# Kernel optimization log

Measured on AMD Instinct MI355X. Metric: run time of the kernel, lower is better.

## Reference

```python
import jax, jax.numpy as jnp
import numpy as np

NUM_USERS = 80000
NUM_ITEMS = 40000
NUM_NODES = NUM_USERS + NUM_ITEMS
LATENT_DIM = 64
N_LAYERS = 3
ALPHA = 0.8
E_POS = 3_000_000
E_NEG = 1_500_000
E_PATH = 2_000_000
N_PATHS = 6


def _make_edges(rng, n_edges, n_nodes):
    # sample keys, dedupe so COO is coalesced (distinct (row,col) pairs)
    keys = rng.integers(0, n_nodes * n_nodes, size=int(n_edges * 1.05), dtype=np.int64)
    keys = np.unique(keys)[:n_edges]
    assert keys.shape[0] == n_edges
    row = (keys // n_nodes).astype(np.int32)
    col = (keys % n_nodes).astype(np.int32)
    return row, col


def setup_inputs() -> dict:
    key = jax.random.key(0)
    k1, k2, k3, k4, k5 = jax.random.split(key, 5)
    rng = np.random.default_rng(0)

    pos_row, pos_col = _make_edges(rng, E_POS, NUM_NODES)
    neg_row, neg_col = _make_edges(rng, E_NEG, NUM_NODES)
    p_row, p_col = _make_edges(rng, E_PATH, NUM_NODES)

    # path membership counts: for each coalesced edge, how many times each of the
    # 6 path matrices contains it (0/1 here); at least one path per edge
    counts = (rng.random((E_PATH, N_PATHS)) < 0.5).astype(np.float32)
    empty = counts.sum(axis=1) == 0
    counts[empty, 0] = 1.0

    return {
        "user_emb": 0.1 * jax.random.normal(k1, (NUM_USERS, LATENT_DIM), jnp.float32),
        "item_emb": 0.1 * jax.random.normal(k2, (NUM_ITEMS, LATENT_DIM), jnp.float32),
        "theta": jnp.ones((N_PATHS,), jnp.float32) / N_PATHS,
        "pos_row": jnp.asarray(pos_row),
        "pos_col": jnp.asarray(pos_col),
        "pos_val": jax.random.uniform(k3, (E_POS,), jnp.float32, 0.01, 1.0),
        "neg_row": jnp.asarray(neg_row),
        "neg_col": jnp.asarray(neg_col),
        "neg_val": jax.random.uniform(k4, (E_NEG,), jnp.float32, 0.01, 1.0),
        "p_row": jnp.asarray(p_row),
        "p_col": jnp.asarray(p_col),
        "p_counts": jnp.asarray(counts),
    }


def _spmm(row, col, val, x, n_nodes):
    # y = A @ x with A given as COO edge list: gather + segment scatter-add
    return jax.ops.segment_sum(val[:, None] * x[col], row, num_segments=n_nodes)


def reference(user_emb, item_emb, theta, pos_row, pos_col, pos_val,
              neg_row, neg_col, neg_val, p_row, p_col, p_counts):
    n = NUM_NODES

    # ---- build path-weighted matrix (coalesce + sparse row softmax, eq.(2)) ----
    theta_w = jax.nn.softmax(theta)                 # [6]
    vals = p_counts @ theta_w                       # coalesced values per edge [E_path]
    exp_v = jnp.exp(vals)
    row_sums = jax.ops.segment_sum(exp_v, p_row, num_segments=n)
    soft_v = exp_v / (row_sums[p_row] + 1e-12)      # row-level sparse softmax

    # ---- PEE: E_0 = P @ all_emb ----
    all_emb = jnp.concatenate([user_emb, item_emb], axis=0)  # [N, D]
    e = _spmm(p_row, p_col, soft_v, all_emb, n)
    embs = [e]

    # ---- signed propagation ----
    for _ in range(N_LAYERS):
        e_pos = _spmm(pos_row, pos_col, pos_val, e, n)
        e_neg_a = _spmm(neg_row, neg_col, neg_val, e, n)
        e = e_pos + ALPHA * (e - e_neg_a)
        embs.append(e)

    light_out = jnp.mean(jnp.stack(embs, axis=1), axis=1)   # [N, D]
    users = light_out[:NUM_USERS]
    items = light_out[NUM_USERS:]
    return users, items
```

## Files before the change

### kernel.cpp

```cpp
#include <hip/hip_runtime.h>

#define NUM_USERS 80000
#define NUM_ITEMS 40000
#define NUM_NODES 120000
#define DIM 64
#define ALPHA_C 0.8f

typedef unsigned short u16;
typedef unsigned int u32;
typedef int   i2v __attribute__((ext_vector_type(2)));
typedef u32   u4v __attribute__((ext_vector_type(4)));
typedef float f4v __attribute__((ext_vector_type(4)));

__device__ __forceinline__ u16 f2bf(float f) {
    union { float f; u32 i; } v;
    v.f = f;
    u32 i = v.i;
    u32 r = (i + 0x7FFFu + ((i >> 16) & 1u)) >> 16;
    return (u16)r;
}
__device__ __forceinline__ float lo_bf(u32 u) { return __uint_as_float(u << 16); }
__device__ __forceinline__ float hi_bf(u32 u) { return __uint_as_float(u & 0xffff0000u); }

__device__ __forceinline__ void acc8(float* __restrict__ acc, float v, uint4 q) {
    const u32* p = (const u32*)&q;
#pragma unroll
    for (int k = 0; k < 4; ++k) {
        u32 u = p[k];
        acc[2 * k]     = fmaf(v, lo_bf(u), acc[2 * k]);
        acc[2 * k + 1] = fmaf(v, hi_bf(u), acc[2 * k + 1]);
    }
}

__device__ __forceinline__ uint4 ldrow(const u16* __restrict__ x, int c, int li) {
    return *((const uint4*)(x + (size_t)c * DIM) + li);
}

template <bool SUMV>
__device__ __forceinline__ void seg_pipe(const i2v* __restrict__ ep0,
                                         int start, int end,
                                         const u16* __restrict__ x,
                                         int li,
                                         float* __restrict__ acc,
                                         float* __restrict__ vsum) {
    const int n = end - start;
    const i2v* ep = ep0 + start;
    float s = 0.f;
    const int np = n >> 1;
    if (np >= 4) {
        i2v ea0 = ep[0], ea1 = ep[1];
        i2v eb0 = ep[2], eb1 = ep[3];
        i2v ec0 = ep[4], ec1 = ep[5];
        i2v ed0 = ep[6], ed1 = ep[7];
        uint4 xa0 = ldrow(x, ea0.x, li), xa1 = ldrow(x, ea1.x, li);
        uint4 xb0 = ldrow(x, eb0.x, li), xb1 = ldrow(x, eb1.x, li);
        for (int p = 4; p < np; ++p) {
            i2v ee0 = ep[2 * p];
            i2v ee1 = ep[2 * p + 1];
            uint4 xc0 = ldrow(x, ec0.x, li);
            uint4 xc1 = ldrow(x, ec1.x, li);
            float va0 = __int_as_float(ea0.y), va1 = __int_as_float(ea1.y);
            acc8(acc, va0, xa0);
            acc8(acc, va1, xa1);
            if (SUMV) s += va0 + va1;
            ea0 = eb0; ea1 = eb1; eb0 = ec0; eb1 = ec1;
            ec0 = ed0; ec1 = ed1; ed0 = ee0; ed1 = ee1;
            xa0 = xb0; xa1 = xb1; xb0 = xc0; xb1 = xc1;
        }
        uint4 xc0 = ldrow(x, ec0.x, li), xc1 = ldrow(x, ec1.x, li);
        uint4 xd0 = ldrow(x, ed0.x, li), xd1 = ldrow(x, ed1.x, li);
        {
            float va0 = __int_as_float(ea0.y), va1 = __int_as_float(ea1.y);
            acc8(acc, va0, xa0); acc8(acc, va1, xa1);
            if (SUMV) s += va0 + va1;
        }
        {
            float vb0 = __int_as_float(eb0.y), vb1 = __int_as_float(eb1.y);
            acc8(acc, vb0, xb0); acc8(acc, vb1, xb1);
            if (SUMV) s += vb0 + vb1;
        }
        {
            float vc0 = __int_as_float(ec0.y), vc1 = __int_as_float(ec1.y);
            acc8(acc, vc0, xc0); acc8(acc, vc1, xc1);
            if (SUMV) s += vc0 + vc1;
        }
        {
            float vd0 = __int_as_float(ed0.y), vd1 = __int_as_float(ed1.y);
            acc8(acc, vd0, xd0); acc8(acc, vd1, xd1);
            if (SUMV) s += vd0 + vd1;
        }
        if (n & 1) {
            i2v eq = ep[n - 1];
            float v = __int_as_float(eq.y);
            uint4 xq = ldrow(x, eq.x, li);
            acc8(acc, v, xq);
            if (SUMV) s += v;
        }
    } else {
        for (int e = 0; e < n; ++e) {
            i2v eq = ep[e];
            float v = __int_as_float(eq.y);
            uint4 xq = ldrow(x, eq.x, li);
            acc8(acc, v, xq);
            if (SUMV) s += v;
        }
    }
    if (SUMV) *vsum = s;
}

__global__ void k_expv_pack(const float* __restrict__ p_counts,
                            const float* __restrict__ theta,
                            const int* __restrict__ p_col,
                            i2v* __restrict__ pev, int E) {
    int i = blockIdx.x * blockDim.x + threadIdx.x;
    if (i >= E) return;
    float m = -1e30f;
    for (int k = 0; k < 6; ++k) m = fmaxf(m, theta[k]);
    float e[6];
    float s = 0.f;
    for (int k = 0; k < 6; ++k) { e[k] = expf(theta[k] - m); s += e[k]; }
    float w0 = e[0] / s, w1 = e[1] / s, w2 = e[2] / s,
          w3 = e[3] / s, w4 = e[4] / s, w5 = e[5] / s;
    const float* c = p_counts + (size_t)i * 6;
    float v = c[0] * w0 + c[1] * w1 + c[2] * w2 +
              c[3] * w3 + c[4] * w4 + c[5] * w5;
    i2v o;
    o.x = __builtin_nontemporal_load(p_col + i);
    o.y = __float_as_int(expf(v));
    __builtin_nontemporal_store(o, pev + i);
}

__device__ __forceinline__ int lower_bound_v(const int* __restrict__ rows,
                                             int nnz, int r) {
    int lo = 0, hi = nnz;
    while (lo < hi) {
        int mid = (lo + hi) >> 1;
        if (rows[mid] < r) lo = mid + 1; else hi = mid;
    }
    return lo;
}

__global__ void k_row_ptr4(const int* __restrict__ rows_a, int nnz_a, int* __restrict__ pa,
                           const int* __restrict__ rows_b, int nnz_b, int* __restrict__ pb,
                           const int* __restrict__ rows_c, int nnz_c, int* __restrict__ pc,
                           int* __restrict__ pm) {
    int t = blockIdx.x * blockDim.x + threadIdx.x;
    int which = t / (NUM_NODES + 1);
    int r = t - which * (NUM_NODES + 1);
    if (which == 0) pa[r] = lower_bound_v(rows_a, nnz_a, r);
    else if (which == 1) pb[r] = lower_bound_v(rows_b, nnz_b, r);
    else if (which == 2) pc[r] = lower_bound_v(rows_c, nnz_c, r);
    else if (which == 3) pm[r] = lower_bound_v(rows_a, nnz_a, r) +
                                 lower_bound_v(rows_b, nnz_b, r);
}

__global__ void k_cvt(const float* __restrict__ user_emb,
                      const float* __restrict__ item_emb,
                      u16* __restrict__ emb16) {
    int i = blockIdx.x * blockDim.x + threadIdx.x;
    size_t f = (size_t)i * 4;
    const size_t UTOT = (size_t)NUM_USERS * DIM;
    const size_t TOT = (size_t)NUM_NODES * DIM;
    if (f >= TOT) return;
    f4v v = (f < UTOT) ? __builtin_nontemporal_load((const f4v*)(user_emb + f))
                       : __builtin_nontemporal_load((const f4v*)(item_emb + (f - UTOT)));
    ushort4 o;
    o.x = f2bf(v.x); o.y = f2bf(v.y); o.z = f2bf(v.z); o.w = f2bf(v.w);
    *(ushort4*)(emb16 + f) = o;
}

__global__ void k_merge_e(const int* __restrict__ row_p, const int* __restrict__ col_p,
                          const float* __restrict__ val_p,
                          const int* __restrict__ row_n, const int* __restrict__ col_n,
                          const float* __restrict__ val_n,
                          const int* __restrict__ rp_p, const int* __restrict__ rp_n,
                          i2v* __restrict__ mev, int E_pos, int E_tot) {
    int g = blockIdx.x * blockDim.x + threadIdx.x;
    if (g >= E_tot) return;
    if (g < E_pos) {
        int r = __builtin_nontemporal_load(row_p + g);
        i2v e;
        e.x = __builtin_nontemporal_load(col_p + g);
        e.y = __float_as_int(__builtin_nontemporal_load(val_p + g));
        __builtin_nontemporal_store(e, mev + (size_t)g + rp_n[r]);
    } else {
        int i = g - E_pos;
        int r = __builtin_nontemporal_load(row_n + i);
        i2v e;
        e.x = __builtin_nontemporal_load(col_n + i);
        e.y = __float_as_int(-ALPHA_C * __builtin_nontemporal_load(val_n + i));
        __builtin_nontemporal_store(e, mev + (size_t)i + rp_p[r + 1]);
    }
}

__global__ void k_path(const u16* __restrict__ emb16,
                       const i2v* __restrict__ pev,
                       const int* __restrict__ rp,
                       u16* __restrict__ e0) {
    int t = blockIdx.x * blockDim.x + threadIdx.x;
    int row = t >> 3;
    if (row >= NUM_NODES) return;
    int li = threadIdx.x & 7;
    int start = rp[row], end = rp[row + 1];

    float acc[8];
#pragma unroll
    for (int k = 0; k < 8; ++k) acc[k] = 0.f;
    float s = 0.f;

    seg_pipe<true>(pev, start, end, emb16, li, acc, &s);

    float inv = 1.0f / (s + 1e-12f);
    u32 o[4];
#pragma unroll
    for (int k = 0; k < 4; ++k)
        o[k] = (u32)f2bf(acc[2 * k] * inv) | ((u32)f2bf(acc[2 * k + 1] * inv) << 16);
    *((uint4*)(e0 + (size_t)row * DIM) + li) = *(uint4*)o;
}

template <int FINAL>
__global__ void k_layer_t(const u16* __restrict__ e_in,
                          u16* __restrict__ e_out,
                          const u16* __restrict__ e0,
                          const u16* __restrict__ e1,
                          float* __restrict__ out,
                          const int* __restrict__ rp_m,
                          const i2v* __restrict__ mev) {
    int t = blockIdx.x * blockDim.x + threadIdx.x;
    int row = t >> 3;
    if (row >= NUM_NODES) return;
    int li = threadIdx.x & 7;

    uint4 eq = *((const uint4*)(e_in + (size_t)row * DIM) + li);

    float acc[8];
#pragma unroll
    for (int k = 0; k < 8; ++k) acc[k] = 0.f;

    seg_pipe<false>(mev, rp_m[row], rp_m[row + 1], e_in, li, acc, nullptr);

    const u32* ep_ = (const u32*)&eq;
    float res[8];
#pragma unroll
    for (int k = 0; k < 4; ++k) {
        res[2 * k]     = acc[2 * k]     + ALPHA_C * lo_bf(ep_[k]);
        res[2 * k + 1] = acc[2 * k + 1] + ALPHA_C * hi_bf(ep_[k]);
    }

    if (FINAL) {
        u4v q0 = __builtin_nontemporal_load((const u4v*)(e0 + (size_t)row * DIM) + li);
        u4v q1 = __builtin_nontemporal_load((const u4v*)(e1 + (size_t)row * DIM) + li);
        float of[8];
#pragma unroll
        for (int k = 0; k < 4; ++k) {
            float lo = res[2 * k]     + lo_bf(ep_[k]) + lo_bf(q0[k]) + lo_bf(q1[k]);
            float hi = res[2 * k + 1] + hi_bf(ep_[k]) + hi_bf(q0[k]) + hi_bf(q1[k]);
            of[2 * k]     = 0.25f * lo;
            of[2 * k + 1] = 0.25f * hi;
        }
        f4v o0, o1;
        o0.x = of[0]; o0.y = of[1]; o0.z = of[2]; o0.w = of[3];
        o1.x = of[4]; o1.y = of[5]; o1.z = of[6]; o1.w = of[7];
        f4v* sp = (f4v*)(out + (size_t)row * DIM) + li * 2;
        __builtin_nontemporal_store(o0, sp);
        __builtin_nontemporal_store(o1, sp + 1);
    } else {
        u32 o[4];
#pragma unroll
        for (int k = 0; k < 4; ++k)
            o[k] = (u32)f2bf(res[2 * k]) | ((u32)f2bf(res[2 * k + 1]) << 16);
        *((uint4*)(e_out + (size_t)row * DIM) + li) = *(uint4*)o;
    }
}

extern "C" void kernel_launch(void* const* d_in, const int* in_sizes, int n_in,
                              void* d_out, int out_size, void* d_ws, size_t ws_size,
                              hipStream_t stream) {
    const float* user_emb = (const float*)d_in[0];
    const float* item_emb = (const float*)d_in[1];
    const float* theta    = (const float*)d_in[2];
    const int*   pos_row  = (const int*)d_in[3];
    const int*   pos_col  = (const int*)d_in[4];
    const float* pos_val  = (const float*)d_in[5];
    const int*   neg_row  = (const int*)d_in[6];
    const int*   neg_col  = (const int*)d_in[7];
    const float* neg_val  = (const float*)d_in[8];
    const int*   p_row    = (const int*)d_in[9];
    const int*   p_col    = (const int*)d_in[10];
    const float* p_counts = (const float*)d_in[11];
    const int E_pos  = in_sizes[3];
    const int E_neg  = in_sizes[6];
    const int E_path = in_sizes[9];

    char* wsb = (char*)d_ws;
    size_t off = 0;
    auto alloc = [&](size_t bytes) -> void* {
        void* p = wsb + off;
        off = (off + bytes + 255) & ~(size_t)255;
        return p;
    };
    i2v*   pev     = (i2v*)alloc((size_t)E_path * sizeof(i2v));
    int*   rp_pos  = (int*)alloc((size_t)(NUM_NODES + 1) * sizeof(int));
    int*   rp_neg  = (int*)alloc((size_t)(NUM_NODES + 1) * sizeof(int));
    int*   rp_path = (int*)alloc((size_t)(NUM_NODES + 1) * sizeof(int));
    int*   rp_m    = (int*)alloc((size_t)(NUM_NODES + 1) * sizeof(int));
    i2v*   mev     = (i2v*)alloc((size_t)(E_pos + E_neg) * sizeof(i2v));
    u16*   emb16   = (u16*)alloc((size_t)NUM_NODES * DIM * sizeof(u16));
    u16*   e0      = (u16*)alloc((size_t)NUM_NODES * DIM * sizeof(u16));
    u16*   e1      = (u16*)alloc((size_t)NUM_NODES * DIM * sizeof(u16));
    u16*   e2      = emb16;
    float* outp    = (float*)d_out;

    k_expv_pack<<<(E_path + 255) / 256, 256, 0, stream>>>(p_counts, theta, p_col,
                                                          pev, E_path);

    int total_rp = 4 * (NUM_NODES + 1);
    k_row_ptr4<<<(total_rp + 255) / 256, 256, 0, stream>>>(
        pos_row, E_pos, rp_pos, neg_row, E_neg, rp_neg, p_row, E_path, rp_path,
        rp_m);

    int cvt_threads = (NUM_NODES * DIM) / 4;
    k_cvt<<<(cvt_threads + 255) / 256, 256, 0, stream>>>(user_emb, item_emb, emb16);

    int E_tot = E_pos + E_neg;
    k_merge_e<<<(E_tot + 255) / 256, 256, 0, stream>>>(
        pos_row, pos_col, pos_val, neg_row, neg_col, neg_val,
        rp_pos, rp_neg, mev, E_pos, E_tot);

    int row_blocks = (NUM_NODES + 31) / 32;

    k_path<<<row_blocks, 256, 0, stream>>>(emb16, pev, rp_path, e0);
    k_layer_t<0><<<row_blocks, 256, 0, stream>>>(e0, e1, nullptr, nullptr, nullptr,
                                                 rp_m, mev);
    k_layer_t<0><<<row_blocks, 256, 0, stream>>>(e1, e2, nullptr, nullptr, nullptr,
                                                 rp_m, mev);
    k_layer_t<1><<<row_blocks, 256, 0, stream>>>(e2, nullptr, e0, e1, outp,
                                                 rp_m, mev);
}
```

Before: 484.0 us.

## Sort rows by degree so each wavefront processes rows of similar length

Builds a degree histogram, scans it, and scatters per-row metadata (start, end, row id) into degree-sorted order for both the path and merged signed matrices. The SpMM kernels then process rows in this order, so the 8 rows sharing a wavefront have similar nonzero counts and lanes diverge less. This adds three small preprocessing kernels plus atomics. Output writes and self-loads become scattered by row id, which weakens locality.

```diff
diff --git a/kernel.cpp b/kernel.cpp
--- a/kernel.cpp
+++ b/kernel.cpp
@@ -143,8 +143,9 @@
 __global__ void k_row_ptr4(const int* __restrict__ rows_a, int nnz_a, int* __restrict__ pa,
                            const int* __restrict__ rows_b, int nnz_b, int* __restrict__ pb,
                            const int* __restrict__ rows_c, int nnz_c, int* __restrict__ pc,
-                           int* __restrict__ pm) {
-    int t = blockIdx.x * blockDim.x + threadIdx.x;
+                           int* __restrict__ pm, int* __restrict__ bins) {
+    int t = blockIdx.x * blockDim.x + threadIdx.x;
+    if (t < 512) bins[t] = 0;
     int which = t / (NUM_NODES + 1);
     int r = t - which * (NUM_NODES + 1);
     if (which == 0) pa[r] = lower_bound_v(rows_a, nnz_a, r);
@@ -152,6 +153,49 @@
     else if (which == 2) pc[r] = lower_bound_v(rows_c, nnz_c, r);
     else if (which == 3) pm[r] = lower_bound_v(rows_a, nnz_a, r) +
                                  lower_bound_v(rows_b, nnz_b, r);
+}
+
+__global__ void k_deg_hist(const int* __restrict__ rp_m,
+                           const int* __restrict__ rp_p,
+                           int* __restrict__ bins) {
+    int t = blockIdx.x * blockDim.x + threadIdx.x;
+    if (t >= 2 * NUM_NODES) return;
+    int which = t >= NUM_NODES;
+    int r = t - which * NUM_NODES;
+    const int* rp = which ? rp_p : rp_m;
+    int deg = rp[r + 1] - rp[r];
+    int b = deg < 255 ? deg : 255;
+    atomicAdd(bins + which * 256 + b, 1);
+}
+
+__global__ void k_deg_scan(const int* __restrict__ bins,
+                           int* __restrict__ bases) {
+    int w = threadIdx.x;
+    if (w < 2) {
+        int run = 0;
+        for (int b = 0; b < 256; ++b) {
+            bases[w * 256 + b] = run;
+            run += bins[w * 256 + b];
+        }
+    }
+}
+
+__global__ void k_deg_scatter(const int* __restrict__ rp_m,
+                              const int* __restrict__ rp_p,
+                              int* __restrict__ bases,
+                              int4* __restrict__ meta_m,
+                              int4* __restrict__ meta_p) {
+    int t = blockIdx.x * blockDim.x + threadIdx.x;
+    if (t >= 2 * NUM_NODES) return;
+    int which = t >= NUM_NODES;
+    int r = t - which * NUM_NODES;
+    const int* rp = which ? rp_p : rp_m;
+    int s = rp[r], e = rp[r + 1];
+    int deg = e - s;
+    int b = deg < 255 ? deg : 255;
+    int pos = atomicAdd(bases + which * 256 + b, 1);
+    int4 md; md.x = s; md.y = e; md.z = r; md.w = 0;
+    (which ? meta_p : meta_m)[pos] = md;
 }
 
 __global__ void k_cvt(const float* __restrict__ user_emb,
@@ -195,27 +239,27 @@
 
 __global__ void k_path(const u16* __restrict__ emb16,
                        const i2v* __restrict__ pev,
-                       const int* __restrict__ rp,
+                       const int4* __restrict__ meta_p,
                        u16* __restrict__ e0) {
     int t = blockIdx.x * blockDim.x + threadIdx.x;
-    int row = t >> 3;
-    if (row >= NUM_NODES) return;
+    int g = t >> 3;
+    if (g >= NUM_NODES) return;
     int li = threadIdx.x & 7;
-    int start = rp[row], end = rp[row + 1];
+    int4 md = meta_p[g];
 
     float acc[8];
 #pragma unroll
     for (int k = 0; k < 8; ++k) acc[k] = 0.f;
     float s = 0.f;
 
-    seg_pipe<true>(pev, start, end, emb16, li, acc, &s);
+    seg_pipe<true>(pev, md.x, md.y, emb16, li, acc, &s);
 
     float inv = 1.0f / (s + 1e-12f);
     u32 o[4];
 #pragma unroll
     for (int k = 0; k < 4; ++k)
         o[k] = (u32)f2bf(acc[2 * k] * inv) | ((u32)f2bf(acc[2 * k + 1] * inv) << 16);
-    *((uint4*)(e0 + (size_t)row * DIM) + li) = *(uint4*)o;
+    *((uint4*)(e0 + (size_t)md.z * DIM) + li) = *(uint4*)o;
 }
 
 template <int FINAL>
@@ -224,20 +268,21 @@
                           const u16* __restrict__ e0,
                           const u16* __restrict__ e1,
                           float* __restrict__ out,
-                          const int* __restrict__ rp_m,
+                          const int4* __restrict__ meta_m,
                           const i2v* __restrict__ mev) {
     int t = blockIdx.x * blockDim.x + threadIdx.x;
-    int row = t >> 3;
-    if (row >= NUM_NODES) return;
+    int g = t >> 3;
+    if (g >= NUM_NODES) return;
     int li = threadIdx.x & 7;
-
-    uint4 eq = *((const uint4*)(e_in + (size_t)row * DIM) + li);
+    int4 md = meta_m[g];
+
+    uint4 eq = *((const uint4*)(e_in + (size_t)md.z * DIM) + li);
 
     float acc[8];
 #pragma unroll
     for (int k = 0; k < 8; ++k) acc[k] = 0.f;
 
-    seg_pipe<false>(mev, rp_m[row], rp_m[row + 1], e_in, li, acc, nullptr);
+    seg_pipe<false>(mev, md.x, md.y, e_in, li, acc, nullptr);
 
     const u32* ep_ = (const u32*)&eq;
     float res[8];
@@ -248,8 +293,8 @@
     }
 
     if (FINAL) {
-        u4v q0 = __builtin_nontemporal_load((const u4v*)(e0 + (size_t)row * DIM) + li);
-        u4v q1 = __builtin_nontemporal_load((const u4v*)(e1 + (size_t)row * DIM) + li);
+        u4v q0 = __builtin_nontemporal_load((const u4v*)(e0 + (size_t)md.z * DIM) + li);
+        u4v q1 = __builtin_nontemporal_load((const u4v*)(e1 + (size_t)md.z * DIM) + li);
         float of[8];
 #pragma unroll
         for (int k = 0; k < 4; ++k) {
@@ -261,7 +306,7 @@
         f4v o0, o1;
         o0.x = of[0]; o0.y = of[1]; o0.z = of[2]; o0.w = of[3];
         o1.x = of[4]; o1.y = of[5]; o1.z = of[6]; o1.w = of[7];
-        f4v* sp = (f4v*)(out + (size_t)row * DIM) + li * 2;
+        f4v* sp = (f4v*)(out + (size_t)md.z * DIM) + li * 2;
         __builtin_nontemporal_store(o0, sp);
         __builtin_nontemporal_store(o1, sp + 1);
     } else {
@@ -269,7 +314,7 @@
 #pragma unroll
         for (int k = 0; k < 4; ++k)
             o[k] = (u32)f2bf(res[2 * k]) | ((u32)f2bf(res[2 * k + 1]) << 16);
-        *((uint4*)(e_out + (size_t)row * DIM) + li) = *(uint4*)o;
+        *((uint4*)(e_out + (size_t)md.z * DIM) + li) = *(uint4*)o;
     }
 }
 
@@ -304,6 +349,10 @@
     int*   rp_neg  = (int*)alloc((size_t)(NUM_NODES + 1) * sizeof(int));
     int*   rp_path = (int*)alloc((size_t)(NUM_NODES + 1) * sizeof(int));
     int*   rp_m    = (int*)alloc((size_t)(NUM_NODES + 1) * sizeof(int));
+    int*   bins    = (int*)alloc(512 * sizeof(int));
+    int*   bases   = (int*)alloc(512 * sizeof(int));
+    int4*  meta_m  = (int4*)alloc((size_t)NUM_NODES * sizeof(int4));
+    int4*  meta_p  = (int4*)alloc((size_t)NUM_NODES * sizeof(int4));
     i2v*   mev     = (i2v*)alloc((size_t)(E_pos + E_neg) * sizeof(i2v));
     u16*   emb16   = (u16*)alloc((size_t)NUM_NODES * DIM * sizeof(u16));
     u16*   e0      = (u16*)alloc((size_t)NUM_NODES * DIM * sizeof(u16));
@@ -317,7 +366,7 @@
     int total_rp = 4 * (NUM_NODES + 1);
     k_row_ptr4<<<(total_rp + 255) / 256, 256, 0, stream>>>(
         pos_row, E_pos, rp_pos, neg_row, E_neg, rp_neg, p_row, E_path, rp_path,
-        rp_m);
+        rp_m, bins);
 
     int cvt_threads = (NUM_NODES * DIM) / 4;
     k_cvt<<<(cvt_threads + 255) / 256, 256, 0, stream>>>(user_emb, item_emb, emb16);
@@ -327,13 +376,19 @@
         pos_row, pos_col, pos_val, neg_row, neg_col, neg_val,
         rp_pos, rp_neg, mev, E_pos, E_tot);
 
+    int nh = 2 * NUM_NODES;
+    k_deg_hist<<<(nh + 255) / 256, 256, 0, stream>>>(rp_m, rp_path, bins);
+    k_deg_scan<<<1, 64, 0, stream>>>(bins, bases);
+    k_deg_scatter<<<(nh + 255) / 256, 256, 0, stream>>>(rp_m, rp_path, bases,
+                                                        meta_m, meta_p);
+
     int row_blocks = (NUM_NODES + 31) / 32;
 
-    k_path<<<row_blocks, 256, 0, stream>>>(emb16, pev, rp_path, e0);
+    k_path<<<row_blocks, 256, 0, stream>>>(emb16, pev, meta_p, e0);
     k_layer_t<0><<<row_blocks, 256, 0, stream>>>(e0, e1, nullptr, nullptr, nullptr,
-                                                 rp_m, mev);
+                                                 meta_m, mev);
     k_layer_t<0><<<row_blocks, 256, 0, stream>>>(e1, e2, nullptr, nullptr, nullptr,
-                                                 rp_m, mev);
+                                                 meta_m, mev);
     k_layer_t<1><<<row_blocks, 256, 0, stream>>>(e2, nullptr, e0, e1, outp,
-                                                 rp_m, mev);
-}
+                                                 meta_m, mev);
+}
```

Measured after the change: 1.433 ms. 2.96x slower.

## Fuse prep kernels into one launch and deepen gather prefetch pipeline

Applied to the files above, without the earlier changes.

Merges the three independent preprocessing kernels (exp-value packing, bf16 conversion, row-pointer binary search) into a single launch that dispatches work by block index. This removes two kernel launches and lets the three jobs' blocks run concurrently instead of one after another. Separately, the SpMM gather loop now prefetches three edge-pairs of embedding rows ahead instead of two, giving more memory-latency hiding at the cost of extra vector registers and possibly lower occupancy.

```diff
diff --git a/kernel.cpp b/kernel.cpp
--- a/kernel.cpp
+++ b/kernel.cpp
@@ -54,20 +54,20 @@
         i2v ed0 = ep[6], ed1 = ep[7];
         uint4 xa0 = ldrow(x, ea0.x, li), xa1 = ldrow(x, ea1.x, li);
         uint4 xb0 = ldrow(x, eb0.x, li), xb1 = ldrow(x, eb1.x, li);
+        uint4 xc0 = ldrow(x, ec0.x, li), xc1 = ldrow(x, ec1.x, li);
         for (int p = 4; p < np; ++p) {
             i2v ee0 = ep[2 * p];
             i2v ee1 = ep[2 * p + 1];
-            uint4 xc0 = ldrow(x, ec0.x, li);
-            uint4 xc1 = ldrow(x, ec1.x, li);
+            uint4 xd0 = ldrow(x, ed0.x, li);
+            uint4 xd1 = ldrow(x, ed1.x, li);
             float va0 = __int_as_float(ea0.y), va1 = __int_as_float(ea1.y);
             acc8(acc, va0, xa0);
             acc8(acc, va1, xa1);
             if (SUMV) s += va0 + va1;
             ea0 = eb0; ea1 = eb1; eb0 = ec0; eb1 = ec1;
             ec0 = ed0; ec1 = ed1; ed0 = ee0; ed1 = ee1;
-            xa0 = xb0; xa1 = xb1; xb0 = xc0; xb1 = xc1;
-        }
-        uint4 xc0 = ldrow(x, ec0.x, li), xc1 = ldrow(x, ec1.x, li);
+            xa0 = xb0; xa1 = xb1; xb0 = xc0; xb1 = xc1; xc0 = xd0; xc1 = xd1;
+        }
         uint4 xd0 = ldrow(x, ed0.x, li), xd1 = ldrow(x, ed1.x, li);
         {
             float va0 = __int_as_float(ea0.y), va1 = __int_as_float(ea1.y);
@@ -108,28 +108,6 @@
     if (SUMV) *vsum = s;
 }
 
-__global__ void k_expv_pack(const float* __restrict__ p_counts,
-                            const float* __restrict__ theta,
-                            const int* __restrict__ p_col,
-                            i2v* __restrict__ pev, int E) {
-    int i = blockIdx.x * blockDim.x + threadIdx.x;
-    if (i >= E) return;
-    float m = -1e30f;
-    for (int k = 0; k < 6; ++k) m = fmaxf(m, theta[k]);
-    float e[6];
-    float s = 0.f;
-    for (int k = 0; k < 6; ++k) { e[k] = expf(theta[k] - m); s += e[k]; }
-    float w0 = e[0] / s, w1 = e[1] / s, w2 = e[2] / s,
-          w3 = e[3] / s, w4 = e[4] / s, w5 = e[5] / s;
-    const float* c = p_counts + (size_t)i * 6;
-    float v = c[0] * w0 + c[1] * w1 + c[2] * w2 +
-              c[3] * w3 + c[4] * w4 + c[5] * w5;
-    i2v o;
-    o.x = __builtin_nontemporal_load(p_col + i);
-    o.y = __float_as_int(expf(v));
-    __builtin_nontemporal_store(o, pev + i);
-}
-
 __device__ __forceinline__ int lower_bound_v(const int* __restrict__ rows,
                                              int nnz, int r) {
     int lo = 0, hi = nnz;
@@ -140,33 +118,59 @@
     return lo;
 }
 
-__global__ void k_row_ptr4(const int* __restrict__ rows_a, int nnz_a, int* __restrict__ pa,
-                           const int* __restrict__ rows_b, int nnz_b, int* __restrict__ pb,
-                           const int* __restrict__ rows_c, int nnz_c, int* __restrict__ pc,
-                           int* __restrict__ pm) {
-    int t = blockIdx.x * blockDim.x + threadIdx.x;
-    int which = t / (NUM_NODES + 1);
-    int r = t - which * (NUM_NODES + 1);
-    if (which == 0) pa[r] = lower_bound_v(rows_a, nnz_a, r);
-    else if (which == 1) pb[r] = lower_bound_v(rows_b, nnz_b, r);
-    else if (which == 2) pc[r] = lower_bound_v(rows_c, nnz_c, r);
-    else if (which == 3) pm[r] = lower_bound_v(rows_a, nnz_a, r) +
-                                 lower_bound_v(rows_b, nnz_b, r);
-}
-
-__global__ void k_cvt(const float* __restrict__ user_emb,
-                      const float* __restrict__ item_emb,
-                      u16* __restrict__ emb16) {
-    int i = blockIdx.x * blockDim.x + threadIdx.x;
-    size_t f = (size_t)i * 4;
-    const size_t UTOT = (size_t)NUM_USERS * DIM;
-    const size_t TOT = (size_t)NUM_NODES * DIM;
-    if (f >= TOT) return;
-    f4v v = (f < UTOT) ? __builtin_nontemporal_load((const f4v*)(user_emb + f))
-                       : __builtin_nontemporal_load((const f4v*)(item_emb + (f - UTOT)));
-    ushort4 o;
-    o.x = f2bf(v.x); o.y = f2bf(v.y); o.z = f2bf(v.z); o.w = f2bf(v.w);
-    *(ushort4*)(emb16 + f) = o;
+__global__ void k_prep(const float* __restrict__ p_counts,
+                       const float* __restrict__ theta,
+                       const int* __restrict__ p_col,
+                       i2v* __restrict__ pev, int E_path,
+                       const float* __restrict__ user_emb,
+                       const float* __restrict__ item_emb,
+                       u16* __restrict__ emb16,
+                       const int* __restrict__ rows_a, int nnz_a, int* __restrict__ pa,
+                       const int* __restrict__ rows_b, int nnz_b, int* __restrict__ pb,
+                       const int* __restrict__ rows_c, int nnz_c, int* __restrict__ pc,
+                       int* __restrict__ pm,
+                       int nb_expv, int nb_cvt) {
+    int b = blockIdx.x;
+    int tid = threadIdx.x;
+    if (b < nb_expv) {
+        int i = b * 256 + tid;
+        if (i >= E_path) return;
+        float m = -1e30f;
+        for (int k = 0; k < 6; ++k) m = fmaxf(m, theta[k]);
+        float e[6];
+        float s = 0.f;
+        for (int k = 0; k < 6; ++k) { e[k] = expf(theta[k] - m); s += e[k]; }
+        float w0 = e[0] / s, w1 = e[1] / s, w2 = e[2] / s,
+              w3 = e[3] / s, w4 = e[4] / s, w5 = e[5] / s;
+        const float* c = p_counts + (size_t)i * 6;
+        float v = c[0] * w0 + c[1] * w1 + c[2] * w2 +
+                  c[3] * w3 + c[4] * w4 + c[5] * w5;
+        i2v o;
+        o.x = __builtin_nontemporal_load(p_col + i);
+        o.y = __float_as_int(expf(v));
+        __builtin_nontemporal_store(o, pev + i);
+    } else if (b < nb_expv + nb_cvt) {
+        int i = (b - nb_expv) * 256 + tid;
+        size_t f = (size_t)i * 4;
+        const size_t UTOT = (size_t)NUM_USERS * DIM;
+        const size_t TOT = (size_t)NUM_NODES * DIM;
+        if (f >= TOT) return;
+        f4v v = (f < UTOT)
+            ? __builtin_nontemporal_load((const f4v*)(user_emb + f))
+            : __builtin_nontemporal_load((const f4v*)(item_emb + (f - UTOT)));
+        ushort4 o;
+        o.x = f2bf(v.x); o.y = f2bf(v.y); o.z = f2bf(v.z); o.w = f2bf(v.w);
+        *(ushort4*)(emb16 + f) = o;
+    } else {
+        int t = (b - nb_expv - nb_cvt) * 256 + tid;
+        int which = t / (NUM_NODES + 1);
+        int r = t - which * (NUM_NODES + 1);
+        if (which == 0) pa[r] = lower_bound_v(rows_a, nnz_a, r);
+        else if (which == 1) pb[r] = lower_bound_v(rows_b, nnz_b, r);
+        else if (which == 2) pc[r] = lower_bound_v(rows_c, nnz_c, r);
+        else if (which == 3) pm[r] = lower_bound_v(rows_a, nnz_a, r) +
+                                     lower_bound_v(rows_b, nnz_b, r);
+    }
 }
 
 __global__ void k_merge_e(const int* __restrict__ row_p, const int* __restrict__ col_p,
@@ -311,16 +315,14 @@
     u16*   e2      = emb16;
     float* outp    = (float*)d_out;
 
-    k_expv_pack<<<(E_path + 255) / 256, 256, 0, stream>>>(p_counts, theta, p_col,
-                                                          pev, E_path);
-
-    int total_rp = 4 * (NUM_NODES + 1);
-    k_row_ptr4<<<(total_rp + 255) / 256, 256, 0, stream>>>(
+    int nb_expv = (E_path + 255) / 256;
+    int nb_cvt  = ((NUM_NODES * DIM) / 4 + 255) / 256;
+    int nb_rp   = (4 * (NUM_NODES + 1) + 255) / 256;
+    k_prep<<<nb_expv + nb_cvt + nb_rp, 256, 0, stream>>>(
+        p_counts, theta, p_col, pev, E_path,
+        user_emb, item_emb, emb16,
         pos_row, E_pos, rp_pos, neg_row, E_neg, rp_neg, p_row, E_path, rp_path,
-        rp_m);
-
-    int cvt_threads = (NUM_NODES * DIM) / 4;
-    k_cvt<<<(cvt_threads + 255) / 256, 256, 0, stream>>>(user_emb, item_emb, emb16);
+        rp_m, nb_expv, nb_cvt);
 
     int E_tot = E_pos + E_neg;
     k_merge_e<<<(E_tot + 255) / 256, 256, 0, stream>>>(
```

Measured after the change: 480.2 us. About the same (-0.8%).
